# Optimization experiments

Hardware: AMD Instinct MI355X
Metric: run time of the kernel (lower is better)

## Reference

```python
import jax, jax.numpy as jnp
import numpy as np

N_EMBD = 1024
HEAD_SIZE = 128


def setup_inputs() -> dict:
    key = jax.random.key(0)
    k_x, k_w, k_cov, k_b = jax.random.split(key, 4)
    x = jax.random.normal(k_x, (16384, 2, N_EMBD), dtype=jnp.float32)
    # values_proj: nn.Linear(n_embd, head_size, bias=False) -> weight [head_size, n_embd]
    W = jax.random.normal(k_w, (HEAD_SIZE, N_EMBD), dtype=jnp.float32) * (N_EMBD ** -0.5)
    cov = jax.random.normal(k_cov, (HEAD_SIZE, HEAD_SIZE), dtype=jnp.float32) * (HEAD_SIZE ** -0.5)
    bias = jax.random.normal(k_b, (HEAD_SIZE,), dtype=jnp.float32)
    return {"x": x, "W": W, "cov": cov, "bias": bias}


def reference(x, W, cov, bias):
    # x: [B, 2, E]; W: [H, E]; cov: [H, H]; bias: [H]
    values = jnp.einsum('be,he->bh', x[:, 0, :], W)  # [B, H]
    mask = jnp.einsum('be,he->bh', x[:, 1, :], W)    # [B, H]
    # diag_embed(mask) @ cov == mask[:, :, None] * cov  -> [B, H, H]
    coeffs = jax.nn.softmax(mask[:, :, None] * cov[None, :, :], axis=-1)
    # values.unsqueeze(1) @ coeffs + bias, then [:, 0, :]
    out = jnp.einsum('bh,bhk->bk', values, coeffs) + bias
    return out
```

## Files before the change

### kernel.cpp

```cpp
#include <hip/hip_runtime.h>
#include <hip/hip_bf16.h>

#define LOG2E 1.4426950408889634f

typedef __attribute__((ext_vector_type(8))) short frag_ab;
typedef __attribute__((ext_vector_type(4))) float frag_cd;

__device__ inline short f2bf(float f) {
    union { float f; unsigned u; } v; v.f = f;
    unsigned r = v.u + 0x7fffu + ((v.u >> 16) & 1u);
    return (short)(r >> 16);
}

__global__ __launch_bounds__(256) void prep_kernel(const float* __restrict__ W,
                                                   const float* __restrict__ cov,
                                                   short* __restrict__ wbf,
                                                   unsigned short* __restrict__ covh) {
    if (blockIdx.x < 64) {
        int g = blockIdx.x * 256 + threadIdx.x;
        int h = g >> 7;
        int k0 = (g & 127) << 3;
        const float* src = W + h * 1024 + k0;
        float4 w0 = *(const float4*)src;
        float4 w1 = *(const float4*)(src + 4);
        frag_ab af;
        af[0] = f2bf(w0.x); af[1] = f2bf(w0.y); af[2] = f2bf(w0.z); af[3] = f2bf(w0.w);
        af[4] = f2bf(w1.x); af[5] = f2bf(w1.y); af[6] = f2bf(w1.z); af[7] = f2bf(w1.w);
        int c = k0 >> 6, s = (k0 >> 5) & 1, kg = (k0 >> 3) & 3;
        int nt = h >> 4, m = h & 15, lane = kg * 16 + m;
        int dst = (((c * 8 + nt) * 2 + s) * 64 + lane) * 8;
        *(frag_ab*)(wbf + dst) = af;
    } else {
        int t = threadIdx.x;
        int h = t >> 1;
        int k0 = (t & 1) * 64;
        const float* cr = cov + h * 128 + k0;
        int rot = 16 * (h & 3);
        for (int k = 0; k < 64; ++k) {
            float c = cr[k] * LOG2E;
            union { _Float16 hf; unsigned short us; } cu;
            cu.hf = (_Float16)c;
            int p = (k0 + k + rot) & 127;
            covh[h * 128 + p] = cu.us;
        }
    }
}

__global__ __launch_bounds__(256, 2) void fused_kernel(const float* __restrict__ x,
                                                       const short* __restrict__ wbf,
                                                       const unsigned short* __restrict__ covh,
                                                       const float* __restrict__ bias,
                                                       float* __restrict__ out) {
    __shared__ __align__(16) unsigned short cov_s[128 * 128];
    __shared__ __align__(16) float vm_s[4][128][16];

    const int tid = threadIdx.x;

    {
        const float4* cg = (const float4*)covh;
        float4* cl = (float4*)cov_s;
#pragma unroll
        for (int q = 0; q < 8; ++q) cl[q * 256 + tid] = cg[q * 256 + tid];
    }

    const int lane = tid & 63, wave = tid >> 6;
    const int m = lane & 15, kg = lane >> 4;
    const long rowbase = (long)blockIdx.x * 64 + wave * 16;
    const float* xrow = x + (rowbase + m) * 1024 + kg * 8;
    const char* wb = (const char*)wbf + lane * 16;

    frag_cd acc[8];
#pragma unroll
    for (int nt = 0; nt < 8; ++nt) acc[nt] = (frag_cd){0.f, 0.f, 0.f, 0.f};

    frag_ab bfr[2][16];
    float4 aq[3][4];

#pragma unroll
    for (int f = 0; f < 16; ++f) bfr[0][f] = *(const frag_ab*)(wb + f * 1024);
#pragma unroll
    for (int pc = 0; pc < 3; ++pc) {
        const float* xn = xrow + pc * 64;
        aq[pc][0] = *(const float4*)(xn);
        aq[pc][1] = *(const float4*)(xn + 4);
        aq[pc][2] = *(const float4*)(xn + 32);
        aq[pc][3] = *(const float4*)(xn + 36);
    }

#pragma unroll
    for (int c = 0; c < 16; ++c) {
        float4 a0 = aq[c % 3][0], a1 = aq[c % 3][1];
        float4 a2 = aq[c % 3][2], a3 = aq[c % 3][3];
        frag_ab af0, af1;
        af0[0] = f2bf(a0.x); af0[1] = f2bf(a0.y); af0[2] = f2bf(a0.z); af0[3] = f2bf(a0.w);
        af0[4] = f2bf(a1.x); af0[5] = f2bf(a1.y); af0[6] = f2bf(a1.z); af0[7] = f2bf(a1.w);
        af1[0] = f2bf(a2.x); af1[1] = f2bf(a2.y); af1[2] = f2bf(a2.z); af1[3] = f2bf(a2.w);
        af1[4] = f2bf(a3.x); af1[5] = f2bf(a3.y); af1[6] = f2bf(a3.z); af1[7] = f2bf(a3.w);

        if (c < 15) {
            const char* bc = wb + (c + 1) * 16384;
#pragma unroll
            for (int f = 0; f < 16; ++f)
                bfr[(c + 1) & 1][f] = *(const frag_ab*)(bc + f * 1024);
        }
        if (c + 3 < 16) {
            const float* xn = xrow + (c + 3) * 64;
            aq[c % 3][0] = *(const float4*)(xn);
            aq[c % 3][1] = *(const float4*)(xn + 4);
            aq[c % 3][2] = *(const float4*)(xn + 32);
            aq[c % 3][3] = *(const float4*)(xn + 36);
        }

#pragma unroll
        for (int nt = 0; nt < 8; ++nt) {
            acc[nt] = __builtin_amdgcn_mfma_f32_16x16x32_bf16(af0, bfr[c & 1][nt * 2 + 0], acc[nt], 0, 0, 0);
            acc[nt] = __builtin_amdgcn_mfma_f32_16x16x32_bf16(af1, bfr[c & 1][nt * 2 + 1], acc[nt], 0, 0, 0);
        }
    }

#pragma unroll
    for (int nt = 0; nt < 8; ++nt) {
        *(float4*)&vm_s[wave][nt * 16 + m][kg * 4] =
            make_float4(acc[nt][0], acc[nt][1], acc[nt][2], acc[nt][3]);
    }
    __syncthreads();

    const int i = lane >> 4;
    const int j = lane & 15;

    float biasr[8];
#pragma unroll
    for (int s = 0; s < 4; ++s) {
        float2 bp = *(const float2*)(bias + 2 * j + 32 * s);
        biasr[2 * s] = bp.x; biasr[2 * s + 1] = bp.y;
    }
    int colb[4];
#pragma unroll
    for (int s = 0; s < 4; ++s) colb[s] = ((2 * j + 32 * s + 16 * i) & 127) * 2;
    const char* covb = (const char*)cov_s;

#pragma unroll 1
    for (int bb = 0; bb < 8; ++bb) {
        float op[8] = {0.f, 0.f, 0.f, 0.f, 0.f, 0.f, 0.f, 0.f};
#pragma unroll 4
        for (int tt = 0; tt < 32; ++tt) {
            int h = 4 * tt + i;
            float2 vmv = *(const float2*)&vm_s[wave][h][2 * bb];
            float mval = vmv.y;
            int rb = h * 256;
            float p[8];
            float ls = 0.f;
#pragma unroll
            for (int s = 0; s < 4; ++s) {
                unsigned cc = *(const unsigned*)(covb + rb + colb[s]);
                union { unsigned u; _Float16 hx[2]; } cu; cu.u = cc;
                float p0 = __builtin_amdgcn_exp2f(mval * (float)cu.hx[0]);
                float p1 = __builtin_amdgcn_exp2f(mval * (float)cu.hx[1]);
                p[2 * s] = p0; p[2 * s + 1] = p1;
                ls += p0 + p1;
            }
            ls += __shfl_xor(ls, 1, 16);
            ls += __shfl_xor(ls, 2, 16);
            ls += __shfl_xor(ls, 4, 16);
            ls += __shfl_xor(ls, 8, 16);
            float w = vmv.x * __builtin_amdgcn_rcpf(ls);
#pragma unroll
            for (int u = 0; u < 8; ++u) op[u] = fmaf(w, p[u], op[u]);
        }
#pragma unroll
        for (int u = 0; u < 8; ++u) {
            op[u] += __shfl_xor(op[u], 16, 64);
            op[u] += __shfl_xor(op[u], 32, 64);
        }
        if (lane < 16) {
            long b = (long)blockIdx.x * 32 + wave * 8 + bb;
            float* ob = out + b * 128;
#pragma unroll
            for (int s = 0; s < 4; ++s) {
                float2 o2;
                o2.x = op[2 * s] + biasr[2 * s];
                o2.y = op[2 * s + 1] + biasr[2 * s + 1];
                *(float2*)(ob + 2 * j + 32 * s) = o2;
            }
        }
    }
}

extern "C" void kernel_launch(void* const* d_in, const int* in_sizes, int n_in,
                              void* d_out, int out_size, void* d_ws, size_t ws_size,
                              hipStream_t stream) {
    const float* x    = (const float*)d_in[0];
    const float* W    = (const float*)d_in[1];
    const float* cov  = (const float*)d_in[2];
    const float* bias = (const float*)d_in[3];
    float* out = (float*)d_out;

    const int B = in_sizes[0] / (2 * 1024);

    short* wbf = (short*)d_ws;
    unsigned short* covh = (unsigned short*)(wbf + 128 * 1024);

    prep_kernel<<<65, 256, 0, stream>>>(W, cov, wbf, covh);

    const int blocks = (2 * B) / 64;
    fused_kernel<<<blocks, 256, 0, stream>>>(x, wbf, covh, bias, out);
}
```

Before: 287.2 us.

## Split GEMM K across two wave halves and read cov from global

Doubles the block to 512 threads, with two groups of four waves each computing half of the K=1024 reduction, then combining partial sums through shared memory. The 32KB shared cov copy is dropped, and the softmax stage reads the fp16 cov table directly from global/L2 with an unrotated layout. W fragments are loaded right before each MFMA instead of being double-buffered in registers. The aim is higher occupancy and more parallelism per block, at the cost of an extra shared-memory reduction pass and more global loads in the softmax loop.

```diff
diff --git a/kernel.cpp b/kernel.cpp
--- a/kernel.cpp
+++ b/kernel.cpp
@@ -32,52 +32,35 @@
         *(frag_ab*)(wbf + dst) = af;
     } else {
         int t = threadIdx.x;
-        int h = t >> 1;
-        int k0 = (t & 1) * 64;
-        const float* cr = cov + h * 128 + k0;
-        int rot = 16 * (h & 3);
-        for (int k = 0; k < 64; ++k) {
-            float c = cr[k] * LOG2E;
+        for (int e = t; e < 16384; e += 256) {
+            float c = cov[e] * LOG2E;
             union { _Float16 hf; unsigned short us; } cu;
             cu.hf = (_Float16)c;
-            int p = (k0 + k + rot) & 127;
-            covh[h * 128 + p] = cu.us;
+            covh[e] = cu.us;
         }
     }
 }
 
-__global__ __launch_bounds__(256, 2) void fused_kernel(const float* __restrict__ x,
+__global__ __launch_bounds__(512, 4) void fused_kernel(const float* __restrict__ x,
                                                        const short* __restrict__ wbf,
                                                        const unsigned short* __restrict__ covh,
                                                        const float* __restrict__ bias,
                                                        float* __restrict__ out) {
-    __shared__ __align__(16) unsigned short cov_s[128 * 128];
-    __shared__ __align__(16) float vm_s[4][128][16];
+    __shared__ __align__(16) float vm_s[128][68];
 
     const int tid = threadIdx.x;
-
-    {
-        const float4* cg = (const float4*)covh;
-        float4* cl = (float4*)cov_s;
-#pragma unroll
-        for (int q = 0; q < 8; ++q) cl[q * 256 + tid] = cg[q * 256 + tid];
-    }
-
     const int lane = tid & 63, wave = tid >> 6;
+    const int w4 = wave & 3, half = wave >> 2;
     const int m = lane & 15, kg = lane >> 4;
-    const long rowbase = (long)blockIdx.x * 64 + wave * 16;
-    const float* xrow = x + (rowbase + m) * 1024 + kg * 8;
-    const char* wb = (const char*)wbf + lane * 16;
+    const long rowbase = (long)blockIdx.x * 64 + w4 * 16;
+    const float* xrow = x + (rowbase + m) * 1024 + half * 512 + kg * 8;
+    const char* wb = (const char*)wbf + (size_t)half * 8 * 16384 + lane * 16;
 
     frag_cd acc[8];
 #pragma unroll
     for (int nt = 0; nt < 8; ++nt) acc[nt] = (frag_cd){0.f, 0.f, 0.f, 0.f};
 
-    frag_ab bfr[2][16];
     float4 aq[3][4];
-
-#pragma unroll
-    for (int f = 0; f < 16; ++f) bfr[0][f] = *(const frag_ab*)(wb + f * 1024);
 #pragma unroll
     for (int pc = 0; pc < 3; ++pc) {
         const float* xn = xrow + pc * 64;
@@ -88,40 +71,47 @@
     }
 
 #pragma unroll
-    for (int c = 0; c < 16; ++c) {
+    for (int c = 0; c < 8; ++c) {
         float4 a0 = aq[c % 3][0], a1 = aq[c % 3][1];
         float4 a2 = aq[c % 3][2], a3 = aq[c % 3][3];
+        if (c + 3 < 8) {
+            const float* xn = xrow + (c + 3) * 64;
+            aq[c % 3][0] = *(const float4*)(xn);
+            aq[c % 3][1] = *(const float4*)(xn + 4);
+            aq[c % 3][2] = *(const float4*)(xn + 32);
+            aq[c % 3][3] = *(const float4*)(xn + 36);
+        }
         frag_ab af0, af1;
         af0[0] = f2bf(a0.x); af0[1] = f2bf(a0.y); af0[2] = f2bf(a0.z); af0[3] = f2bf(a0.w);
         af0[4] = f2bf(a1.x); af0[5] = f2bf(a1.y); af0[6] = f2bf(a1.z); af0[7] = f2bf(a1.w);
         af1[0] = f2bf(a2.x); af1[1] = f2bf(a2.y); af1[2] = f2bf(a2.z); af1[3] = f2bf(a2.w);
         af1[4] = f2bf(a3.x); af1[5] = f2bf(a3.y); af1[6] = f2bf(a3.z); af1[7] = f2bf(a3.w);
 
-        if (c < 15) {
-            const char* bc = wb + (c + 1) * 16384;
-#pragma unroll
-            for (int f = 0; f < 16; ++f)
-                bfr[(c + 1) & 1][f] = *(const frag_ab*)(bc + f * 1024);
-        }
-        if (c + 3 < 16) {
-            const float* xn = xrow + (c + 3) * 64;
-            aq[c % 3][0] = *(const float4*)(xn);
-            aq[c % 3][1] = *(const float4*)(xn + 4);
-            aq[c % 3][2] = *(const float4*)(xn + 32);
-            aq[c % 3][3] = *(const float4*)(xn + 36);
-        }
-
+        const char* bc = wb + c * 16384;
 #pragma unroll
         for (int nt = 0; nt < 8; ++nt) {
-            acc[nt] = __builtin_amdgcn_mfma_f32_16x16x32_bf16(af0, bfr[c & 1][nt * 2 + 0], acc[nt], 0, 0, 0);
-            acc[nt] = __builtin_amdgcn_mfma_f32_16x16x32_bf16(af1, bfr[c & 1][nt * 2 + 1], acc[nt], 0, 0, 0);
+            frag_ab bf0 = *(const frag_ab*)(bc + (nt * 2 + 0) * 1024);
+            frag_ab bf1 = *(const frag_ab*)(bc + (nt * 2 + 1) * 1024);
+            acc[nt] = __builtin_amdgcn_mfma_f32_16x16x32_bf16(af0, bf0, acc[nt], 0, 0, 0);
+            acc[nt] = __builtin_amdgcn_mfma_f32_16x16x32_bf16(af1, bf1, acc[nt], 0, 0, 0);
         }
     }
 
+    if (half == 0) {
 #pragma unroll
-    for (int nt = 0; nt < 8; ++nt) {
-        *(float4*)&vm_s[wave][nt * 16 + m][kg * 4] =
-            make_float4(acc[nt][0], acc[nt][1], acc[nt][2], acc[nt][3]);
+        for (int nt = 0; nt < 8; ++nt)
+            *(float4*)&vm_s[nt * 16 + m][w4 * 16 + kg * 4] =
+                make_float4(acc[nt][0], acc[nt][1], acc[nt][2], acc[nt][3]);
+    }
+    __syncthreads();
+    if (half == 1) {
+#pragma unroll
+        for (int nt = 0; nt < 8; ++nt) {
+            float4* p = (float4*)&vm_s[nt * 16 + m][w4 * 16 + kg * 4];
+            float4 v = *p;
+            v.x += acc[nt][0]; v.y += acc[nt][1]; v.z += acc[nt][2]; v.w += acc[nt][3];
+            *p = v;
+        }
     }
     __syncthreads();
 
@@ -134,25 +124,22 @@
         float2 bp = *(const float2*)(bias + 2 * j + 32 * s);
         biasr[2 * s] = bp.x; biasr[2 * s + 1] = bp.y;
     }
-    int colb[4];
-#pragma unroll
-    for (int s = 0; s < 4; ++s) colb[s] = ((2 * j + 32 * s + 16 * i) & 127) * 2;
-    const char* covb = (const char*)cov_s;
 
 #pragma unroll 1
-    for (int bb = 0; bb < 8; ++bb) {
+    for (int q = 0; q < 4; ++q) {
+        const int bl = wave * 4 + q;
         float op[8] = {0.f, 0.f, 0.f, 0.f, 0.f, 0.f, 0.f, 0.f};
 #pragma unroll 4
         for (int tt = 0; tt < 32; ++tt) {
             int h = 4 * tt + i;
-            float2 vmv = *(const float2*)&vm_s[wave][h][2 * bb];
+            float2 vmv = *(const float2*)&vm_s[h][2 * bl];
             float mval = vmv.y;
-            int rb = h * 256;
+            const unsigned short* cr = covh + h * 128 + 2 * j;
             float p[8];
             float ls = 0.f;
 #pragma unroll
             for (int s = 0; s < 4; ++s) {
-                unsigned cc = *(const unsigned*)(covb + rb + colb[s]);
+                unsigned cc = *(const unsigned*)(cr + 32 * s);
                 union { unsigned u; _Float16 hx[2]; } cu; cu.u = cc;
                 float p0 = __builtin_amdgcn_exp2f(mval * (float)cu.hx[0]);
                 float p1 = __builtin_amdgcn_exp2f(mval * (float)cu.hx[1]);
@@ -173,7 +160,7 @@
             op[u] += __shfl_xor(op[u], 32, 64);
         }
         if (lane < 16) {
-            long b = (long)blockIdx.x * 32 + wave * 8 + bb;
+            long b = (long)blockIdx.x * 32 + bl;
             float* ob = out + b * 128;
 #pragma unroll
             for (int s = 0; s < 4; ++s) {
@@ -203,5 +190,5 @@
     prep_kernel<<<65, 256, 0, stream>>>(W, cov, wbf, covh);
 
     const int blocks = (2 * B) / 64;
-    fused_kernel<<<blocks, 256, 0, stream>>>(x, wbf, covh, bias, out);
+    fused_kernel<<<blocks, 512, 0, stream>>>(x, wbf, covh, bias, out);
 }
```

New measurement: 276.6 us. 3.7% less time.
